# Optimization experiments

Measured on AMD Instinct MI355X. Metric: run time of the kernel, lower is better.

## Reference

```python
import jax, jax.numpy as jnp
import numpy as np

C = 128; HEADS = 8; GH = 32; GW = 32; B = 8; PD = 8  # PD = (dim//4)//4

def _conv(x, w, pad, dil=1, groups=1):
    return jax.lax.conv_general_dilated(
        x, w, (1, 1), [(pad[0], pad[0]), (pad[1], pad[1])],
        rhs_dilation=(dil, dil),
        dimension_numbers=('NCHW', 'OIHW', 'NCHW'),
        feature_group_count=groups)

def _lrelu(t):
    return jnp.where(t >= 0, t, 0.1 * t)

def _ln(t, g, b, eps=1e-5):
    m = jnp.mean(t, -1, keepdims=True)
    v = jnp.var(t, -1, keepdims=True)
    return (t - m) * jax.lax.rsqrt(v + eps) * g + b

def setup_inputs():
    rng = np.random.RandomState(0)
    f = lambda *s: jnp.asarray((rng.randn(*s) * 0.05).astype(np.float32))
    ones = lambda n: jnp.ones((n,), jnp.float32)
    zeros = lambda n: jnp.zeros((n,), jnp.float32)
    # Swin-style relative position index over the (GH, GW) group
    coords = np.stack(np.meshgrid(np.arange(GH), np.arange(GW), indexing='ij')).reshape(2, -1)
    rel = (coords[:, :, None] - coords[:, None, :]).transpose(1, 2, 0)
    rel[..., 0] += GH - 1; rel[..., 1] += GW - 1; rel[..., 0] *= 2 * GW - 1
    rel_idx = jnp.asarray(rel.sum(-1).astype(np.int32))  # [N, N]
    biases = np.stack(np.meshgrid(np.arange(1 - GH, GH), np.arange(1 - GW, GW), indexing='ij'))
    biases = jnp.asarray(biases.reshape(2, -1).T.astype(np.float32))  # [(2GH-1)*(2GW-1), 2]
    return dict(
        x=jnp.asarray(rng.rand(B, C, GH, GW).astype(np.float32)),
        conv1_w=f(C, C, 3, 3), conv2_w=f(C, C, 3, 3), conv3_w=f(C, C, 3, 3),
        convt_w=f(C, 3, 1, 1),
        rba_w=f(C, C, 3, 1), rba_b=zeros(C), rbb_w=f(C, C, 1, 3), rbb_b=zeros(C),
        pp_w=f(PD, 2), pp_b=zeros(PD),
        l1_g=ones(PD), l1_b=zeros(PD), l1_w=f(PD, PD), l1_b2=zeros(PD),
        l2_g=ones(PD), l2_b=zeros(PD), l2_w=f(PD, PD), l2_b2=zeros(PD),
        l3_g=ones(PD), l3_b=zeros(PD), l3_w=f(HEADS, PD), l3_b2=zeros(HEADS),
        qk_w=f(2 * C, C), qk_b=zeros(2 * C),
        v_w=f(C, C), v_b=zeros(C),
        proj_w=f(C, C), proj_b=zeros(C),
        fc1_w=f(C, C), fc1_b=zeros(C), fc2_w=f(C, C), fc2_b=zeros(C),
        biases=biases, rel_idx=rel_idx,
    )

def reference(x, conv1_w, conv2_w, conv3_w, convt_w, rba_w, rba_b, rbb_w, rbb_b,
              pp_w, pp_b, l1_g, l1_b, l1_w, l1_b2, l2_g, l2_b, l2_w, l2_b2,
              l3_g, l3_b, l3_w, l3_b2, qk_w, qk_b, v_w, v_b, proj_w, proj_b,
              fc1_w, fc1_b, fc2_w, fc2_b, biases, rel_idx):
    Bn, Cc, Hh, Ww = x.shape
    N = Hh * Ww
    hd = Cc // HEADS
    # FeaExtract: ResASPP (3 dilated 3x3 convs, grouped 1x1 merge) + residual
    b1 = _lrelu(_conv(x, conv1_w, (1, 1)))
    b2 = _lrelu(_conv(x, conv2_w, (3, 3), dil=3))
    b3 = _lrelu(_conv(x, conv3_w, (5, 5), dil=5))
    a = _conv(jnp.concatenate([b1, b2, b3], 1), convt_w, (0, 0), groups=Cc) + x
    # RB: (3,1) conv -> lrelu -> (1,3) conv + residual
    r = _lrelu(_conv(a, rba_w, (1, 0)) + rba_b[None, :, None, None])
    r = _conv(r, rbb_w, (0, 1)) + rbb_b[None, :, None, None]
    o0 = r + a
    # original uses in-place clamp_, so o0 is clamped before flattening
    o0 = jnp.clip(o0, 0.0, 1.0)
    E = o0.reshape(Bn, Cc, N).transpose(0, 2, 1)  # [B, N, C]
    qk = E @ qk_w.T + qk_b  # [B, N, 2C]
    q = qk[..., :Cc].reshape(Bn, N, HEADS, hd).transpose(0, 2, 1, 3)
    k = qk[..., Cc:].reshape(Bn, N, HEADS, hd).transpose(0, 2, 1, 3)
    v = (E @ v_w.T + v_b).reshape(Bn, N, HEADS, hd).transpose(0, 2, 1, 3)
    attn = jnp.einsum('bhid,bhjd->bhij', q * (hd ** -0.5), k)
    # DynamicPosBias MLP (residual=False): Linear(2,pd) -> [LN,ReLU,Linear] x2 -> LN,ReLU,Linear(pd,heads)
    p = biases @ pp_w.T + pp_b
    p = jax.nn.relu(_ln(p, l1_g, l1_b)) @ l1_w.T + l1_b2
    p = jax.nn.relu(_ln(p, l2_g, l2_b)) @ l2_w.T + l2_b2
    p = jax.nn.relu(_ln(p, l3_g, l3_b)) @ l3_w.T + l3_b2  # [L, heads]
    rpb = p[rel_idx]  # gather -> [N, N, heads]
    attn = attn + rpb.transpose(2, 0, 1)[None]
    attn = jax.nn.softmax(attn, axis=-1)
    y = jnp.einsum('bhij,bhjd->bhid', attn, v).transpose(0, 2, 1, 3).reshape(Bn, N, Cc) + E
    x_proj = y @ proj_w.T + proj_b
    h = jax.nn.gelu(x_proj @ fc1_w.T + fc1_b, approximate=False)
    return (h @ fc2_w.T + fc2_b) + y
```

## Files before the change

### kernel.cpp

```cpp
#include <hip/hip_runtime.h>
#include <hip/hip_bf16.h>

typedef __hip_bfloat16 bf16;
typedef __bf16 bf16x8 __attribute__((ext_vector_type(8)));
typedef float f32x4 __attribute__((ext_vector_type(4)));
typedef __fp16 f16x2 __attribute__((ext_vector_type(2)));
typedef __fp16 f16x4 __attribute__((ext_vector_type(4)));

#define Lb 3969
#define LOG2E 1.4426950408889634f
#define EXP2(x) __builtin_amdgcn_exp2f(x)

#define XP_F   0
#define WF_F   903168
#define WR_F   1124352
#define WG_F   1173504
#define BH_F   1222656
#define QKV_F  1222656
#define AP_F   2795520
#define YT_F   2795520
#define EB_F   3352576
#define RPB_F  3876864
#define FLAG_F 3908616
#define RT_F   3908624
#define VT_F   4924432

__device__ __forceinline__ float b2f(bf16 v) { return __bfloat162float(v); }
__device__ __forceinline__ bf16 f2b(float v) { return __float2bfloat16(v); }

template <typename T> __device__ __forceinline__ float ldw(const void* p, int i);
template <> __device__ __forceinline__ float ldw<bf16>(const void* p, int i) {
  return __bfloat162float(((const bf16*)p)[i]);
}
template <> __device__ __forceinline__ float ldw<float>(const void* p, int i) {
  return ((const float*)p)[i];
}
template <typename T> __device__ __forceinline__ void stw(void* p, size_t i, float v);
template <> __device__ __forceinline__ void stw<bf16>(void* p, size_t i, float v) {
  ((bf16*)p)[i] = __float2bfloat16(v);
}
template <> __device__ __forceinline__ void stw<float>(void* p, size_t i, float v) {
  ((float*)p)[i] = v;
}

__device__ __forceinline__ unsigned pkh(float a, float b) {
  f16x2 t = __builtin_amdgcn_cvt_pkrtz(a, b);
  return *(unsigned*)&t;
}

__device__ __forceinline__ bool detect_local(const unsigned* x) {
  int lane = threadIdx.x & 63;
  int cnt = 0;
#pragma unroll
  for (int k = 0; k < 4; ++k) {
    unsigned lo = x[lane + 64 * k] & 0xFFFFu;
    cnt += (lo >= 0x3C00u && lo < 0x3F80u) ? 1 : 0;
  }
#pragma unroll
  for (int off = 1; off < 64; off <<= 1) cnt += __shfl_xor(cnt, off);
  return cnt >= 128;
}

template <typename T>
__device__ void wprep_all_body(const void* w1, const void* w2, const void* w3,
                               const void* rba_w, const void* rbb_w,
                               const void* qk_w, const void* v_w,
                               const void* proj_w, const void* fc1_w,
                               const void* fc2_w, bf16* __restrict__ Wf,
                               bf16* __restrict__ Wr, bf16* __restrict__ Wg)
{
  int tid = blockIdx.x * 256 + threadIdx.x;
  int lane = tid & 63, li = lane & 15, quad = lane >> 4;
  if (tid < 55296) {
    int mt = (tid >> 6) & 7;
    int Kc = (tid >> 9) & 3;
    int rem = tid >> 11;
    int t = rem % 9;
    int br = rem / 9;
    const void* w = (br == 0 ? w1 : (br == 1 ? w2 : w3));
    int o = mt * 16 + li;
    int ci0 = Kc * 32 + quad * 8;
#pragma unroll
    for (int j = 0; j < 8; ++j)
      Wf[(size_t)tid * 8 + j] = f2b(ldw<T>(w, (o * 128 + ci0 + j) * 9 + t));
  } else {
    int u = tid - 55296;
    if (u < 12288) {
      int Kc = (u >> 6) & 3, mt = (u >> 8) & 7, q = u >> 11;
      const void* w = (q >= 3) ? rbb_w : rba_w;
      int t = q % 3;
#pragma unroll
      for (int j = 0; j < 8; ++j)
        Wr[(size_t)u * 8 + j] =
            f2b(ldw<T>(w, ((mt * 16 + li) * 128 + Kc * 32 + quad * 8 + j) * 3 + t));
    } else if (u < 24576) {
      int g = u - 12288;
      int Kc = (g >> 6) & 3, mtg = g >> 8;
      const void* w; int mrow; float sc = 1.f;
      if (mtg < 16)      { w = qk_w;   mrow = mtg * 16;
                           if (mtg < 8) sc = 0.25f * LOG2E; }
      else if (mtg < 24) { w = v_w;    mrow = (mtg - 16) * 16; }
      else if (mtg < 32) { w = proj_w; mrow = (mtg - 24) * 16; }
      else if (mtg < 40) { w = fc1_w;  mrow = (mtg - 32) * 16; }
      else               { w = fc2_w;  mrow = (mtg - 40) * 16; }
#pragma unroll
      for (int j = 0; j < 8; ++j)
        Wg[(size_t)g * 8 + j] =
            f2b(sc * ldw<T>(w, (mrow + li) * 128 + Kc * 32 + quad * 8 + j));
    }
  }
}

template <typename T>
__device__ void nhwc_body(const void* x, bf16* __restrict__ xp,
                          bf16 (*tile)[128], int bid)
{
  const int b = bid >> 5;
  const int row = bid & 31;
  const int t = threadIdx.x;
  const size_t bbase = (size_t)b * 42 * 42 * 128;
  const bf16x8 z = (bf16x8){};

  if (t < 160) {
    int side = t / 80;
    int off = (t % 80) * 8;
    *(bf16x8*)&xp[bbase + ((size_t)(row + 5) * 42 + side * 37) * 128 + off] = z;
  }
  {
    int zr = (row < 5) ? row : ((row >= 27) ? row + 10 : -1);
    if (zr >= 0) {
      size_t base = bbase + (size_t)zr * 42 * 128;
      for (int k = t; k < 672; k += 256) *(bf16x8*)&xp[base + k * 8] = z;
    }
  }

  {
    int ci = t >> 1, half = t & 1;
#pragma unroll
    for (int j = 0; j < 16; ++j) {
      int px = half * 16 + j;
      tile[px][ci] = f2b(ldw<T>(x, ((size_t)b * 128 + ci) * 1024 + row * 32 + px));
    }
  }
  __syncthreads();
  {
    int px = t >> 3, c0 = (t & 7) * 16;
    bf16* dst = xp + (bbase + ((size_t)(row + 5) * 42 + (px + 5)) * 128 + c0);
#pragma unroll
    for (int j = 0; j < 16; ++j) dst[j] = tile[px][c0 + j];
  }
}

__global__ __launch_bounds__(256) void prep_kernel(
    const unsigned* x, const void* w1, const void* w2, const void* w3,
    const void* rba_w, const void* rbb_w, const void* qk_w, const void* v_w,
    const void* proj_w, const void* fc1_w, const void* fc2_w,
    bf16* Wf, bf16* Wr, bf16* Wg, bf16* xp, int* flag)
{
  __shared__ bf16 tile[32][128];
  bool isbf = detect_local(x);
  if (blockIdx.x < 312) {
    if (blockIdx.x == 0 && threadIdx.x == 0) *flag = isbf ? 1 : 0;
    if (isbf) wprep_all_body<bf16>(w1, w2, w3, rba_w, rbb_w, qk_w, v_w, proj_w,
                                   fc1_w, fc2_w, Wf, Wr, Wg);
    else      wprep_all_body<float>(w1, w2, w3, rba_w, rbb_w, qk_w, v_w, proj_w,
                                    fc1_w, fc2_w, Wf, Wr, Wg);
  } else {
    int bid = blockIdx.x - 312;
    if (isbf) nhwc_body<bf16>(x, xp, tile, bid);
    else      nhwc_body<float>(x, xp, tile, bid);
  }
}

__global__ __launch_bounds__(256) void aspp2_kernel(
    const bf16* __restrict__ xp, const bf16* __restrict__ Wf,
    bf16* __restrict__ bh)
{
  const int nt_ = blockIdx.x, br = blockIdx.y >> 1, mh = blockIdx.y & 1;
  const int bb = blockIdx.z;
  const int w = threadIdx.x >> 6, lane = threadIdx.x & 63;
  const int quad = lane >> 4, li = lane & 15;
  const int d = (br == 0 ? 1 : (br == 1 ? 3 : 5));
  const int pxw = nt_ * 64 + w * 16;
  const int y = pxw >> 5, xb = pxw & 31;

  f32x4 acc[4] = {};
  const bf16* Wbase = Wf + (size_t)br * 18432 * 8 + (size_t)mh * 4 * 64 * 8;

  for (int t = 0; t < 9; ++t) {
    const int dy = (t / 3 - 1) * d, dx = (t % 3 - 1) * d;
    const bf16* Asite =
        xp + (((size_t)bb * 42 + (y + 5 + dy)) * 42 + (xb + li + 5 + dx)) * 128;
    const bf16* Wt = Wbase + (size_t)t * 2048 * 8;
#pragma unroll
    for (int Kc = 0; Kc < 4; ++Kc) {
      bf16x8 afrag = *(const bf16x8*)(Asite + Kc * 32 + quad * 8);
      const bf16* Wk = Wt + (size_t)Kc * 512 * 8 + (size_t)lane * 8;
#pragma unroll
      for (int mt = 0; mt < 4; ++mt) {
        bf16x8 wfrag = *(const bf16x8*)(Wk + (size_t)mt * 64 * 8);
        acc[mt] = __builtin_amdgcn_mfma_f32_16x16x32_bf16(afrag, wfrag, acc[mt],
                                                          0, 0, 0);
      }
    }
  }
#pragma unroll
  for (int mt = 0; mt < 4; ++mt)
#pragma unroll
    for (int r = 0; r < 4; ++r) {
      int px = pxw + quad * 4 + r;
      bh[((size_t)bb * 1024 + px) * 384 + br * 128 + (mh * 4 + mt) * 16 + li] =
          f2b(acc[mt][r]);
    }
}

template <typename T>
__device__ void merge2_body(const bf16* __restrict__ xp, const void* wt,
                            const bf16* __restrict__ bh, bf16* __restrict__ ap,
                            float* cw)
{
  const int b = blockIdx.y, px0 = blockIdx.x * 32;
  const bf16x8 z = (bf16x8){};
  if (blockIdx.x == 0) {
    size_t base = ((size_t)b * 34 + 0) * 32 * 128;
    for (int k = threadIdx.x; k < 512; k += 256) *(bf16x8*)&ap[base + k * 8] = z;
  } else if (blockIdx.x == 31) {
    size_t base = ((size_t)b * 34 + 33) * 32 * 128;
    for (int k = threadIdx.x; k < 512; k += 256) *(bf16x8*)&ap[base + k * 8] = z;
  }
  for (int i = threadIdx.x; i < 384; i += 256) cw[i] = ldw<T>(wt, i);
  __syncthreads();
  const int pxl = threadIdx.x >> 3, og = threadIdx.x & 7;
  const int px = px0 + pxl, o0 = og * 16;
  const int y = px >> 5, x = px & 31;
  const bf16* brow = bh + ((size_t)b * 1024 + px) * 384 + o0 * 3;
  const bf16* xrow = xp + (((size_t)b * 42 + y + 5) * 42 + x + 5) * 128 + o0;
  bf16* arow = ap + (((size_t)b * 34 + y + 1) * 32 + x) * 128 + o0;

  bf16 bl[48], xl[16], ol[16];
#pragma unroll
  for (int k = 0; k < 6; ++k) *(bf16x8*)&bl[k * 8] = *(const bf16x8*)&brow[k * 8];
  *(bf16x8*)&xl[0] = *(const bf16x8*)&xrow[0];
  *(bf16x8*)&xl[8] = *(const bf16x8*)&xrow[8];
#pragma unroll
  for (int j = 0; j < 16; ++j) {
    float v = b2f(xl[j]);
#pragma unroll
    for (int i = 0; i < 3; ++i) {
      float t = b2f(bl[j * 3 + i]);
      v += cw[(o0 + j) * 3 + i] * (t >= 0.f ? t : 0.1f * t);
    }
    ol[j] = f2b(v);
  }
  *(bf16x8*)&arow[0] = *(bf16x8*)&ol[0];
  *(bf16x8*)&arow[8] = *(bf16x8*)&ol[8];
}

__global__ __launch_bounds__(256) void merge2_kernel(
    const bf16* xp, const void* wt, const bf16* bh, bf16* ap, const int* flag)
{
  __shared__ float cw[384];
  if (*flag) merge2_body<bf16>(xp, wt, bh, ap, cw);
  else       merge2_body<float>(xp, wt, bh, ap, cw);
}

template <typename T>
__device__ void rbf_body(const bf16* __restrict__ ap, const bf16* __restrict__ Wr,
                         const void* rba_b, const void* rbb_b,
                         bf16* __restrict__ Eb, bf16 (*r1row)[136])
{
  const int y = blockIdx.x, b = blockIdx.y;
  const int w = threadIdx.x >> 6, lane = threadIdx.x & 63;
  const int mh = w & 1, xb = (w >> 1) * 16;
  const int quad = lane >> 4, li = lane & 15;

  if (threadIdx.x < 128) {
    r1row[0][threadIdx.x] = f2b(0.f);
    r1row[33][threadIdx.x] = f2b(0.f);
  }

  f32x4 acc[4] = {};
#pragma unroll
  for (int t = 0; t < 3; ++t) {
    const bf16* Asite = ap + (((size_t)b * 34 + y + t) * 32 + xb + li) * 128;
#pragma unroll
    for (int Kc = 0; Kc < 4; ++Kc) {
      bf16x8 afrag = *(const bf16x8*)(Asite + Kc * 32 + quad * 8);
#pragma unroll
      for (int mt = 0; mt < 4; ++mt) {
        int f = (t * 8 + mh * 4 + mt) * 4 + Kc;
        bf16x8 wfrag = *(const bf16x8*)(Wr + ((size_t)f * 64 + lane) * 8);
        acc[mt] = __builtin_amdgcn_mfma_f32_16x16x32_bf16(afrag, wfrag, acc[mt],
                                                          0, 0, 0);
      }
    }
  }
#pragma unroll
  for (int mt = 0; mt < 4; ++mt) {
    int o = (mh * 4 + mt) * 16 + li;
    float bv = ldw<T>(rba_b, o);
#pragma unroll
    for (int r = 0; r < 4; ++r) {
      int x = xb + quad * 4 + r;
      float v = acc[mt][r] + bv;
      r1row[x + 1][o] = f2b(v >= 0.f ? v : 0.1f * v);
    }
  }
  __syncthreads();

  f32x4 acc2[4] = {};
#pragma unroll
  for (int t = 0; t < 3; ++t) {
#pragma unroll
    for (int Kc = 0; Kc < 4; ++Kc) {
      bf16x8 afrag = *(const bf16x8*)&r1row[xb + li + t][Kc * 32 + quad * 8];
#pragma unroll
      for (int mt = 0; mt < 4; ++mt) {
        int f = ((3 + t) * 8 + mh * 4 + mt) * 4 + Kc;
        bf16x8 wfrag = *(const bf16x8*)(Wr + ((size_t)f * 64 + lane) * 8);
        acc2[mt] = __builtin_amdgcn_mfma_f32_16x16x32_bf16(afrag, wfrag,
                                                           acc2[mt], 0, 0, 0);
      }
    }
  }
#pragma unroll
  for (int mt = 0; mt < 4; ++mt) {
    int o = (mh * 4 + mt) * 16 + li;
    float bv = ldw<T>(rbb_b, o);
#pragma unroll
    for (int r = 0; r < 4; ++r) {
      int x = xb + quad * 4 + r;
      float v = acc2[mt][r] + bv +
                b2f(ap[(((size_t)b * 34 + y + 1) * 32 + x) * 128 + o]);
      v = fminf(fmaxf(v, 0.f), 1.f);
      Eb[((size_t)b * 1024 + y * 32 + x) * 128 + o] = f2b(v);
    }
  }
}

__global__ __launch_bounds__(256) void rbf_kernel(
    const bf16* ap, const bf16* Wr, const void* rba_b, const void* rbb_b,
    bf16* Eb, const int* flag)
{
  __shared__ bf16 r1row[34][136];
  if (*flag) rbf_body<bf16>(ap, Wr, rba_b, rbb_b, Eb, r1row);
  else       rbf_body<float>(ap, Wr, rba_b, rbb_b, Eb, r1row);
}

template <typename T>
__device__ __forceinline__ void ln_relu8(const float* t, float* u,
                                         const void* g, const void* bb)
{
  float m = 0.f;
#pragma unroll
  for (int k = 0; k < 8; ++k) m += t[k];
  m *= 0.125f;
  float v = 0.f;
#pragma unroll
  for (int k = 0; k < 8; ++k) { float d = t[k] - m; v += d * d; }
  v *= 0.125f;
  float r = rsqrtf(v + 1e-5f);
#pragma unroll
  for (int k = 0; k < 8; ++k) {
    float val = (t[k] - m) * r * ldw<T>(g, k) + ldw<T>(bb, k);
    u[k] = val > 0.f ? val : 0.f;
  }
}

template <typename T>
__device__ __forceinline__ float dpb_one(
    int r, int h, const void* biases, const void* pp_w, const void* pp_b,
    const void* l1_g, const void* l1_b, const void* l1_w, const void* l1_b2,
    const void* l2_g, const void* l2_b, const void* l2_w, const void* l2_b2,
    const void* l3_g, const void* l3_b, const void* l3_w, const void* l3_b2)
{
  float b0 = ldw<T>(biases, r * 2), b1 = ldw<T>(biases, r * 2 + 1);
  float t[8], u[8];
#pragma unroll
  for (int j = 0; j < 8; ++j)
    t[j] = b0 * ldw<T>(pp_w, j * 2) + b1 * ldw<T>(pp_w, j * 2 + 1) +
           ldw<T>(pp_b, j);
  ln_relu8<T>(t, u, l1_g, l1_b);
#pragma unroll
  for (int j = 0; j < 8; ++j) {
    float s = ldw<T>(l1_b2, j);
#pragma unroll
    for (int k = 0; k < 8; ++k) s += u[k] * ldw<T>(l1_w, j * 8 + k);
    t[j] = s;
  }
  ln_relu8<T>(t, u, l2_g, l2_b);
#pragma unroll
  for (int j = 0; j < 8; ++j) {
    float s = ldw<T>(l2_b2, j);
#pragma unroll
    for (int k = 0; k < 8; ++k) s += u[k] * ldw<T>(l2_w, j * 8 + k);
    t[j] = s;
  }
  ln_relu8<T>(t, u, l3_g, l3_b);
  float s = ldw<T>(l3_b2, h);
#pragma unroll
  for (int k = 0; k < 8; ++k) s += u[k] * ldw<T>(l3_w, h * 8 + k);
  return s;
}

template <typename T>
__device__ void dpbrt_body(
    const void* biases, const void* pp_w, const void* pp_b, const void* l1_g,
    const void* l1_b, const void* l1_w, const void* l1_b2, const void* l2_g,
    const void* l2_b, const void* l2_w, const void* l2_b2, const void* l3_g,
    const void* l3_b, const void* l3_w, const void* l3_b2,
    float* __restrict__ RTf, float (*rpl)[47])
{
  const int tt = blockIdx.x, h = blockIdx.y;
  const int t = tt >> 1, p = tt & 1;
  const int lane = threadIdx.x, quad = lane >> 4, li = lane & 15;

  for (int e = lane; e < 94; e += 64) {
    int row = t + e / 47;
    int col = p * 16 + e % 47;
    rpl[e / 47][e % 47] =
        dpb_one<T>(row * 63 + col, h, biases, pp_w, pp_b, l1_g, l1_b, l1_w,
                   l1_b2, l2_g, l2_b, l2_w, l2_b2, l3_g, l3_b, l3_w, l3_b2) *
        LOG2E;
  }
  __syncthreads();

  float* dst = RTf + ((size_t)(h * 124 + tt) * 4) * 256 + lane * 4;
#pragma unroll
  for (int mt = 0; mt < 4; ++mt) {
    f32x4 v;
#pragma unroll
    for (int r = 0; r < 4; ++r) {
      int j = mt * 16 + quad * 4 + r;
      v[r] = rpl[1 - (j >> 5)][li - (j & 31) + 31];
    }
    *(f32x4*)(dst + mt * 256) = v;
  }
}

__global__ __launch_bounds__(64) void dpbrt_kernel(
    const void* biases, const void* pp_w, const void* pp_b, const void* l1_g,
    const void* l1_b, const void* l1_w, const void* l1_b2, const void* l2_g,
    const void* l2_b, const void* l2_w, const void* l2_b2, const void* l3_g,
    const void* l3_b, const void* l3_w, const void* l3_b2, float* RTf,
    const int* flag)
{
  __shared__ float rpl[2][47];
  if (*flag)
    dpbrt_body<bf16>(biases, pp_w, pp_b, l1_g, l1_b, l1_w, l1_b2, l2_g, l2_b,
                     l2_w, l2_b2, l3_g, l3_b, l3_w, l3_b2, RTf, rpl);
  else
    dpbrt_body<float>(biases, pp_w, pp_b, l1_g, l1_b, l1_w, l1_b2, l2_g, l2_b,
                      l2_w, l2_b2, l3_g, l3_b, l3_w, l3_b2, RTf, rpl);
}

template <typename T>
__device__ void qkv_body(const bf16* __restrict__ Eb, const bf16* __restrict__ Wg,
                         const void* qk_b, const void* v_b,
                         bf16* __restrict__ QKV, uint2* __restrict__ VTh)
{
  const int grp = blockIdx.y, b = blockIdx.z;
  const int w = threadIdx.x >> 6, lane = threadIdx.x & 63;
  const int quad = lane >> 4, li = lane & 15;
  const int pxw = blockIdx.x * 64 + w * 16;
  bf16x8 ef[4];
#pragma unroll
  for (int Kc = 0; Kc < 4; ++Kc)
    ef[Kc] = *(const bf16x8*)&Eb[((size_t)b * 1024 + pxw + li) * 128 + Kc * 32 +
                                 quad * 8];
  f32x4 acc[8] = {};
#pragma unroll
  for (int nt = 0; nt < 8; ++nt) {
    int g = grp * 8 + nt;
#pragma unroll
    for (int Kc = 0; Kc < 4; ++Kc) {
      bf16x8 wf = *(const bf16x8*)&Wg[(((size_t)g * 4 + Kc) * 64 + lane) * 8];
      acc[nt] = __builtin_amdgcn_mfma_f32_16x16x32_bf16(ef[Kc], wf, acc[nt],
                                                        0, 0, 0);
    }
  }
  if (grp < 2) {
#pragma unroll
    for (int nt = 0; nt < 8; ++nt) {
      int g = grp * 8 + nt;
      int o = g * 16 + li;
      float bv = (g < 8) ? (0.25f * LOG2E) * ldw<T>(qk_b, o) : ldw<T>(qk_b, o);
#pragma unroll
      for (int r = 0; r < 4; ++r) {
        int px = pxw + quad * 4 + r;
        QKV[((size_t)b * 1024 + px) * 384 + o] = f2b(acc[nt][r] + bv);
      }
    }
  } else {
#pragma unroll
    for (int nt = 0; nt < 8; ++nt) {
      int hh = nt;
      float bv = ldw<T>(v_b, nt * 16 + li);
      uint2 pu;
      pu.x = pkh(acc[nt][0] + bv, acc[nt][1] + bv);
      pu.y = pkh(acc[nt][2] + bv, acc[nt][3] + bv);
      VTh[(((size_t)(b * 8 + hh) * 16 + blockIdx.x) * 4 + w) * 64 + lane] = pu;
    }
  }
}

__global__ __launch_bounds__(256) void qkv_kernel(
    const bf16* Eb, const bf16* Wg, const void* qk_b, const void* v_b,
    bf16* QKV, uint2* VTh, const int* flag)
{
  if (*flag) qkv_body<bf16>(Eb, Wg, qk_b, v_b, QKV, VTh);
  else       qkv_body<float>(Eb, Wg, qk_b, v_b, QKV, VTh);
}

template <typename T>
__device__ void mlpf_body(const bf16* __restrict__ Yt, const bf16* __restrict__ Wg,
                          const void* proj_b, const void* fc1_b,
                          const void* fc2_b, void* out,
                          bf16 (*buf0)[136], bf16 (*buf1)[136])
{
  const int w = threadIdx.x >> 6, lane = threadIdx.x & 63;
  const int quad = lane >> 4, li = lane & 15;
  const size_t row0 = (size_t)blockIdx.x * 16;

  bf16x8 ef[4];
  f32x4 acc[2];

#pragma unroll
  for (int Kc = 0; Kc < 4; ++Kc)
    ef[Kc] = *(const bf16x8*)&Yt[(row0 + li) * 128 + Kc * 32 + quad * 8];
  acc[0] = (f32x4){}; acc[1] = (f32x4){};
#pragma unroll
  for (int j = 0; j < 2; ++j) {
    int g = 24 + w * 2 + j;
#pragma unroll
    for (int Kc = 0; Kc < 4; ++Kc) {
      bf16x8 wf = *(const bf16x8*)&Wg[(((size_t)g * 4 + Kc) * 64 + lane) * 8];
      acc[j] = __builtin_amdgcn_mfma_f32_16x16x32_bf16(ef[Kc], wf, acc[j],
                                                       0, 0, 0);
    }
  }
#pragma unroll
  for (int j = 0; j < 2; ++j) {
    int o = (w * 2 + j) * 16 + li;
    float bv = ldw<T>(proj_b, o);
#pragma unroll
    for (int r = 0; r < 4; ++r)
      buf0[quad * 4 + r][o] = f2b(acc[j][r] + bv);
  }
  __syncthreads();

#pragma unroll
  for (int Kc = 0; Kc < 4; ++Kc)
    ef[Kc] = *(const bf16x8*)&buf0[li][Kc * 32 + quad * 8];
  acc[0] = (f32x4){}; acc[1] = (f32x4){};
#pragma unroll
  for (int j = 0; j < 2; ++j) {
    int g = 32 + w * 2 + j;
#pragma unroll
    for (int Kc = 0; Kc < 4; ++Kc) {
      bf16x8 wf = *(const bf16x8*)&Wg[(((size_t)g * 4 + Kc) * 64 + lane) * 8];
      acc[j] = __builtin_amdgcn_mfma_f32_16x16x32_bf16(ef[Kc], wf, acc[j],
                                                       0, 0, 0);
    }
  }
#pragma unroll
  for (int j = 0; j < 2; ++j) {
    int o = (w * 2 + j) * 16 + li;
    float bv = ldw<T>(fc1_b, o);
#pragma unroll
    for (int r = 0; r < 4; ++r) {
      float v = acc[j][r] + bv;
      v = 0.5f * v * (1.f + erff(v * 0.70710678118f));
      buf1[quad * 4 + r][o] = f2b(v);
    }
  }
  __syncthreads();

#pragma unroll
  for (int Kc = 0; Kc < 4; ++Kc)
    ef[Kc] = *(const bf16x8*)&buf1[li][Kc * 32 + quad * 8];
  acc[0] = (f32x4){}; acc[1] = (f32x4){};
#pragma unroll
  for (int j = 0; j < 2; ++j) {
    int g = 40 + w * 2 + j;
#pragma unroll
    for (int Kc = 0; Kc < 4; ++Kc) {
      bf16x8 wf = *(const bf16x8*)&Wg[(((size_t)g * 4 + Kc) * 64 + lane) * 8];
      acc[j] = __builtin_amdgcn_mfma_f32_16x16x32_bf16(ef[Kc], wf, acc[j],
                                                       0, 0, 0);
    }
  }
#pragma unroll
  for (int j = 0; j < 2; ++j) {
    int o = (w * 2 + j) * 16 + li;
    float bv = ldw<T>(fc2_b, o);
#pragma unroll
    for (int r = 0; r < 4; ++r) {
      size_t oidx = (row0 + quad * 4 + r) * 128 + o;
      float v = acc[j][r] + bv + b2f(Yt[oidx]);
      stw<T>(out, oidx, v);
    }
  }
}

__global__ __launch_bounds__(256) void mlpf_kernel(
    const bf16* Yt, const bf16* Wg, const void* proj_b, const void* fc1_b,
    const void* fc2_b, void* out, const int* flag)
{
  __shared__ bf16 buf0[16][136];
  __shared__ bf16 buf1[16][136];
  if (*flag) mlpf_body<bf16>(Yt, Wg, proj_b, fc1_b, fc2_b, out, buf0, buf1);
  else       mlpf_body<float>(Yt, Wg, proj_b, fc1_b, fc2_b, out, buf0, buf1);
}

__global__ __launch_bounds__(256, 4) void attn_kernel(
    const bf16* __restrict__ QKV, const bf16* __restrict__ Eb,
    const float* __restrict__ RTf, const uint2* __restrict__ VTh,
    bf16* __restrict__ Yt)
{
  const int qt = blockIdx.x * 4 + (threadIdx.x >> 6);
  const int hh = blockIdx.y;
  const int b = blockIdx.z;

  const int lane = threadIdx.x & 63;
  const int quad = lane >> 4, li = lane & 15;
  const int qb = qt * 16;

  const bf16* QKVb = QKV + (size_t)b * 1024 * 384;
  const uint2* VTb = VTh + (size_t)(b * 8 + hh) * 4096;
  const float* RTh = RTf + (size_t)hh * 124 * 1024;

  bf16x8 qf = (bf16x8){};
  if (quad < 2)
    qf = *(const bf16x8*)&QKVb[(size_t)(qb + li) * 384 + hh * 16 + quad * 8];

  f32x4 Oa = {}, Ob = {};
  float m_st = -1e30f, l_ln = 0.f;
  const int sbase = (lane & 48) + ((lane >> 2) & 12);

  struct Buf { bf16x8 kf[4]; f32x4 cin[4]; uint2 vb[4]; };
  Buf bA, bB;

  auto LOAD = [&](Buf& bf, int c) {
    const int c0 = c * 64;
    const int tt = ((qt >> 1) - 2 * c + 30) * 2 + (qt & 1);
    const float* rtp = RTh + (size_t)tt * 1024 + lane * 4;
#pragma unroll
    for (int mt = 0; mt < 4; ++mt) {
      bf.cin[mt] = *(const f32x4*)(rtp + mt * 256);
      bf.kf[mt] = (bf16x8){};
      if (quad < 2)
        bf.kf[mt] = *(const bf16x8*)&QKVb[(size_t)(c0 + mt * 16 + li) * 384 +
                                          128 + hh * 16 + quad * 8];
      bf.vb[mt] = VTb[(size_t)(c * 4 + mt) * 64 + lane];
    }
  };

  auto STEP = [&](const Buf& bf) {
    f32x4 sT[4];
#pragma unroll
    for (int mt = 0; mt < 4; ++mt)
      sT[mt] = __builtin_amdgcn_mfma_f32_16x16x32_bf16(bf.kf[mt], qf,
                                                       bf.cin[mt], 0, 0, 0);

    float m0 = fmaxf(fmaxf(sT[0][0], sT[0][1]), fmaxf(sT[0][2], sT[0][3]));
    float m1 = fmaxf(fmaxf(sT[1][0], sT[1][1]), fmaxf(sT[1][2], sT[1][3]));
    float m2 = fmaxf(fmaxf(sT[2][0], sT[2][1]), fmaxf(sT[2][2], sT[2][3]));
    float m3 = fmaxf(fmaxf(sT[3][0], sT[3][1]), fmaxf(sT[3][2], sT[3][3]));
    float lmax = fmaxf(fmaxf(m0, m1), fmaxf(m2, m3));

    if (!__all(lmax <= m_st + 11.5f)) {
      float cm = fmaxf(lmax, __shfl_xor(lmax, 16));
      cm = fmaxf(cm, __shfl_xor(cm, 32));
      float mn = fmaxf(m_st, cm);
      float al = EXP2(m_st - mn);
      m_st = mn;
      l_ln *= al;
#pragma unroll
      for (int r = 0; r < 4; ++r) {
        float a = __shfl(al, sbase + r);
        Oa[r] *= a;
        Ob[r] *= a;
      }
    }

#pragma unroll
    for (int mt = 0; mt < 4; ++mt)
#pragma unroll
      for (int r = 0; r < 4; ++r) sT[mt][r] = EXP2(sT[mt][r] - m_st);

    float s0 = (sT[0][0] + sT[0][1]) + (sT[0][2] + sT[0][3]);
    float s1 = (sT[1][0] + sT[1][1]) + (sT[1][2] + sT[1][3]);
    float s2 = (sT[2][0] + sT[2][1]) + (sT[2][2] + sT[2][3]);
    float s3 = (sT[3][0] + sT[3][1]) + (sT[3][2] + sT[3][3]);
    l_ln += (s0 + s1) + (s2 + s3);

#pragma unroll
    for (int mt = 0; mt < 4; ++mt) {
      union { unsigned u[2]; f16x4 h4; } pu;
      pu.u[0] = pkh(sT[mt][0], sT[mt][1]);
      pu.u[1] = pkh(sT[mt][2], sT[mt][3]);
      union { uint2 u; f16x4 h; } vu;
      vu.u = bf.vb[mt];
      if (mt & 2)
        Ob = __builtin_amdgcn_mfma_f32_16x16x16f16(pu.h4, vu.h, Ob, 0, 0, 0);
      else
        Oa = __builtin_amdgcn_mfma_f32_16x16x16f16(pu.h4, vu.h, Oa, 0, 0, 0);
    }
  };

  LOAD(bA, 0);
  for (int c = 0; c < 16; c += 2) {
    LOAD(bB, c + 1);
    STEP(bA);
    if (c + 2 < 16) LOAD(bA, c + 2);
    STEP(bB);
  }

  float l_st = l_ln + __shfl_xor(l_ln, 16);
  l_st += __shfl_xor(l_st, 32);

  f32x4 O_;
#pragma unroll
  for (int r = 0; r < 4; ++r) O_[r] = Oa[r] + Ob[r];

  const bf16* Ebp = Eb + (size_t)b * 1024 * 128 + hh * 16 + li;
  bf16* Ytp = Yt + (size_t)b * 1024 * 128 + hh * 16 + li;
#pragma unroll
  for (int r = 0; r < 4; ++r) {
    float lb = __shfl(l_st, sbase + r);
    int qrow = qb + quad * 4 + r;
    Ytp[(size_t)qrow * 128] =
        f2b(O_[r] / lb + b2f(Ebp[(size_t)qrow * 128]));
  }
}

extern "C" void kernel_launch(void* const* d_in, const int* in_sizes, int n_in,
                              void* d_out, int out_size, void* d_ws,
                              size_t ws_size, hipStream_t stream)
{
  (void)in_sizes; (void)n_in; (void)out_size; (void)ws_size;
  const void* x       = d_in[0];
  const void* conv1_w = d_in[1];
  const void* conv2_w = d_in[2];
  const void* conv3_w = d_in[3];
  const void* convt_w = d_in[4];
  const void* rba_w   = d_in[5];
  const void* rba_b   = d_in[6];
  const void* rbb_w   = d_in[7];
  const void* rbb_b   = d_in[8];
  const void* pp_w    = d_in[9];
  const void* pp_b    = d_in[10];
  const void* l1_g    = d_in[11];
  const void* l1_b    = d_in[12];
  const void* l1_w    = d_in[13];
  const void* l1_b2   = d_in[14];
  const void* l2_g    = d_in[15];
  const void* l2_b    = d_in[16];
  const void* l2_w    = d_in[17];
  const void* l2_b2   = d_in[18];
  const void* l3_g    = d_in[19];
  const void* l3_b    = d_in[20];
  const void* l3_w    = d_in[21];
  const void* l3_b2   = d_in[22];
  const void* qk_w    = d_in[23];
  const void* qk_b    = d_in[24];
  const void* v_w     = d_in[25];
  const void* v_b     = d_in[26];
  const void* proj_w  = d_in[27];
  const void* proj_b  = d_in[28];
  const void* fc1_w   = d_in[29];
  const void* fc1_b   = d_in[30];
  const void* fc2_w   = d_in[31];
  const void* fc2_b   = d_in[32];
  const void* biases  = d_in[33];

  float* ws   = (float*)d_ws;
  bf16*  xp   = (bf16*)(ws + XP_F);
  bf16*  Wf   = (bf16*)(ws + WF_F);
  bf16*  Wr   = (bf16*)(ws + WR_F);
  bf16*  Wg   = (bf16*)(ws + WG_F);
  bf16*  bh   = (bf16*)(ws + BH_F);
  bf16*  QKV  = (bf16*)(ws + QKV_F);
  bf16*  ap   = (bf16*)(ws + AP_F);
  bf16*  Yt   = (bf16*)(ws + YT_F);
  bf16*  Eb   = (bf16*)(ws + EB_F);
  int*   flag = (int*)(ws + FLAG_F);
  float* RTf  = ws + RT_F;
  uint2* VTh  = (uint2*)(ws + VT_F);

  prep_kernel<<<568, 256, 0, stream>>>(
      (const unsigned*)x, conv1_w, conv2_w, conv3_w, rba_w, rbb_w, qk_w, v_w,
      proj_w, fc1_w, fc2_w, Wf, Wr, Wg, xp, flag);
  aspp2_kernel<<<dim3(16, 6, 8), 256, 0, stream>>>(xp, Wf, bh);
  merge2_kernel<<<dim3(32, 8), 256, 0, stream>>>(xp, convt_w, bh, ap, flag);
  rbf_kernel<<<dim3(32, 8), 256, 0, stream>>>(ap, Wr, rba_b, rbb_b, Eb, flag);
  dpbrt_kernel<<<dim3(124, 8), 64, 0, stream>>>(
      biases, pp_w, pp_b, l1_g, l1_b, l1_w, l1_b2, l2_g, l2_b, l2_w, l2_b2,
      l3_g, l3_b, l3_w, l3_b2, RTf, flag);
  qkv_kernel<<<dim3(16, 3, 8), 256, 0, stream>>>(Eb, Wg, qk_b, v_b, QKV, VTh,
                                                 flag);
  attn_kernel<<<dim3(16, 8, 8), 256, 0, stream>>>(QKV, Eb, RTf, VTh, Yt);
  mlpf_kernel<<<512, 256, 0, stream>>>(Yt, Wg, proj_b, fc1_b, fc2_b, d_out,
                                       flag);
}
```

Measured before the change: 229.3 us.

## Fuse ASPP conv with merge and fold position-bias MLP into prep kernel

```diff
diff --git a/kernel.cpp b/kernel.cpp
--- a/kernel.cpp
+++ b/kernel.cpp
@@ -15,12 +15,10 @@
 #define WF_F   903168
 #define WR_F   1124352
 #define WG_F   1173504
-#define BH_F   1222656
 #define QKV_F  1222656
 #define AP_F   2795520
 #define YT_F   2795520
 #define EB_F   3352576
-#define RPB_F  3876864
 #define FLAG_F 3908616
 #define RT_F   3908624
 #define VT_F   4924432
@@ -59,6 +57,62 @@
 #pragma unroll
   for (int off = 1; off < 64; off <<= 1) cnt += __shfl_xor(cnt, off);
   return cnt >= 128;
+}
+
+template <typename T>
+__device__ __forceinline__ void ln_relu8(const float* t, float* u,
+                                         const void* g, const void* bb)
+{
+  float m = 0.f;
+#pragma unroll
+  for (int k = 0; k < 8; ++k) m += t[k];
+  m *= 0.125f;
+  float v = 0.f;
+#pragma unroll
+  for (int k = 0; k < 8; ++k) { float d = t[k] - m; v += d * d; }
+  v *= 0.125f;
+  float r = rsqrtf(v + 1e-5f);
+#pragma unroll
+  for (int k = 0; k < 8; ++k) {
+    float val = (t[k] - m) * r * ldw<T>(g, k) + ldw<T>(bb, k);
+    u[k] = val > 0.f ? val : 0.f;
+  }
+}
+
+template <typename T>
+__device__ __forceinline__ float dpb_one(
+    int r, int h, const void* biases, const void* pp_w, const void* pp_b,
+    const void* l1_g, const void* l1_b, const void* l1_w, const void* l1_b2,
+    const void* l2_g, const void* l2_b, const void* l2_w, const void* l2_b2,
+    const void* l3_g, const void* l3_b, const void* l3_w, const void* l3_b2)
+{
+  float b0 = ldw<T>(biases, r * 2), b1 = ldw<T>(biases, r * 2 + 1);
+  float t[8], u[8];
+#pragma unroll
+  for (int j = 0; j < 8; ++j)
+    t[j] = b0 * ldw<T>(pp_w, j * 2) + b1 * ldw<T>(pp_w, j * 2 + 1) +
+           ldw<T>(pp_b, j);
+  ln_relu8<T>(t, u, l1_g, l1_b);
+#pragma unroll
+  for (int j = 0; j < 8; ++j) {
+    float s = ldw<T>(l1_b2, j);
+#pragma unroll
+    for (int k = 0; k < 8; ++k) s += u[k] * ldw<T>(l1_w, j * 8 + k);
+    t[j] = s;
+  }
+  ln_relu8<T>(t, u, l2_g, l2_b);
+#pragma unroll
+  for (int j = 0; j < 8; ++j) {
+    float s = ldw<T>(l2_b2, j);
+#pragma unroll
+    for (int k = 0; k < 8; ++k) s += u[k] * ldw<T>(l2_w, j * 8 + k);
+    t[j] = s;
+  }
+  ln_relu8<T>(t, u, l3_g, l3_b);
+  float s = ldw<T>(l3_b2, h);
+#pragma unroll
+  for (int k = 0; k < 8; ++k) s += u[k] * ldw<T>(l3_w, h * 8 + k);
+  return s;
 }
 
 template <typename T>
@@ -151,13 +205,50 @@
   }
 }
 
+template <typename T>
+__device__ void dpbrt_wave(
+    int tt, int h, int lane, const void* biases, const void* pp_w,
+    const void* pp_b, const void* l1_g, const void* l1_b, const void* l1_w,
+    const void* l1_b2, const void* l2_g, const void* l2_b, const void* l2_w,
+    const void* l2_b2, const void* l3_g, const void* l3_b, const void* l3_w,
+    const void* l3_b2, float* __restrict__ RTf, float (*rp)[47])
+{
+  const int t = tt >> 1, p = tt & 1;
+  const int quad = lane >> 4, li = lane & 15;
+  for (int e = lane; e < 94; e += 64) {
+    int row = t + e / 47;
+    int col = p * 16 + e % 47;
+    rp[e / 47][e % 47] =
+        dpb_one<T>(row * 63 + col, h, biases, pp_w, pp_b, l1_g, l1_b, l1_w,
+                   l1_b2, l2_g, l2_b, l2_w, l2_b2, l3_g, l3_b, l3_w, l3_b2) *
+        LOG2E;
+  }
+  __syncthreads();
+  float* dst = RTf + ((size_t)(h * 124 + tt) * 4) * 256 + lane * 4;
+#pragma unroll
+  for (int mt = 0; mt < 4; ++mt) {
+    f32x4 v;
+#pragma unroll
+    for (int r = 0; r < 4; ++r) {
+      int j = mt * 16 + quad * 4 + r;
+      v[r] = rp[1 - (j >> 5)][li - (j & 31) + 31];
+    }
+    *(f32x4*)(dst + mt * 256) = v;
+  }
+}
+
 __global__ __launch_bounds__(256) void prep_kernel(
     const unsigned* x, const void* w1, const void* w2, const void* w3,
     const void* rba_w, const void* rbb_w, const void* qk_w, const void* v_w,
     const void* proj_w, const void* fc1_w, const void* fc2_w,
-    bf16* Wf, bf16* Wr, bf16* Wg, bf16* xp, int* flag)
+    bf16* Wf, bf16* Wr, bf16* Wg, bf16* xp, int* flag,
+    const void* biases, const void* pp_w, const void* pp_b, const void* l1_g,
+    const void* l1_b, const void* l1_w, const void* l1_b2, const void* l2_g,
+    const void* l2_b, const void* l2_w, const void* l2_b2, const void* l3_g,
+    const void* l3_b, const void* l3_w, const void* l3_b2, float* RTf)
 {
   __shared__ bf16 tile[32][128];
+  __shared__ float rpl[4][2][47];
   bool isbf = detect_local(x);
   if (blockIdx.x < 312) {
     if (blockIdx.x == 0 && threadIdx.x == 0) *flag = isbf ? 1 : 0;
@@ -165,103 +256,112 @@
                                    fc1_w, fc2_w, Wf, Wr, Wg);
     else      wprep_all_body<float>(w1, w2, w3, rba_w, rbb_w, qk_w, v_w, proj_w,
                                     fc1_w, fc2_w, Wf, Wr, Wg);
-  } else {
+  } else if (blockIdx.x < 568) {
     int bid = blockIdx.x - 312;
     if (isbf) nhwc_body<bf16>(x, xp, tile, bid);
     else      nhwc_body<float>(x, xp, tile, bid);
-  }
-}
-
-__global__ __launch_bounds__(256) void aspp2_kernel(
-    const bf16* __restrict__ xp, const bf16* __restrict__ Wf,
-    bf16* __restrict__ bh)
-{
-  const int nt_ = blockIdx.x, br = blockIdx.y >> 1, mh = blockIdx.y & 1;
-  const int bb = blockIdx.z;
+  } else {
+    int wv = threadIdx.x >> 6, lane = threadIdx.x & 63;
+    int idx = (blockIdx.x - 568) * 4 + wv;
+    int tt = idx % 124, h = idx / 124;
+    if (isbf)
+      dpbrt_wave<bf16>(tt, h, lane, biases, pp_w, pp_b, l1_g, l1_b, l1_w,
+                       l1_b2, l2_g, l2_b, l2_w, l2_b2, l3_g, l3_b, l3_w,
+                       l3_b2, RTf, rpl[wv]);
+    else
+      dpbrt_wave<float>(tt, h, lane, biases, pp_w, pp_b, l1_g, l1_b, l1_w,
+                        l1_b2, l2_g, l2_b, l2_w, l2_b2, l3_g, l3_b, l3_w,
+                        l3_b2, RTf, rpl[wv]);
+  }
+}
+
+#define ASPP_SEG(BR, M8, DIL)                                                  \
+  {                                                                            \
+    for (int t = 0; t < 9; ++t) {                                              \
+      const int dy = (t / 3 - 1) * (DIL), dx = (t % 3 - 1) * (DIL);            \
+      const bf16* Asite =                                                      \
+          xp + (((size_t)bb * 42 + (y + 5 + dy)) * 42 + (xb + li + 5 + dx)) *  \
+                   128;                                                        \
+      const bf16* Wt2 = Wf + (((size_t)(BR)*9 + t) * 4) * 512 * 8;             \
+      _Pragma("unroll") for (int Kc = 0; Kc < 4; ++Kc) {                       \
+        bf16x8 afrag = *(const bf16x8*)(Asite + Kc * 32 + quad * 8);           \
+        const bf16* Wk = Wt2 + (size_t)Kc * 512 * 8 + (size_t)lane * 8;        \
+        _Pragma("unroll") for (int m = 0; m < 4; ++m) {                        \
+          bf16x8 wfrag = *(const bf16x8*)(Wk + (size_t)((M8) + m) * 64 * 8);   \
+          acc[m] = __builtin_amdgcn_mfma_f32_16x16x32_bf16(afrag, wfrag,       \
+                                                           acc[m], 0, 0, 0);   \
+        }                                                                      \
+      }                                                                        \
+    }                                                                          \
+  }
+
+template <typename T>
+__device__ void aspp_merge_body(const bf16* __restrict__ xp,
+                                const bf16* __restrict__ Wf, const void* wt,
+                                bf16* __restrict__ ap, bf16 (*conc)[200],
+                                float* cw)
+{
+  const int nt_ = blockIdx.x, mh = blockIdx.y, bb = blockIdx.z;
   const int w = threadIdx.x >> 6, lane = threadIdx.x & 63;
   const int quad = lane >> 4, li = lane & 15;
-  const int d = (br == 0 ? 1 : (br == 1 ? 3 : 5));
-  const int pxw = nt_ * 64 + w * 16;
+  const int pxw = nt_ * 16;
   const int y = pxw >> 5, xb = pxw & 31;
 
+  if (mh == 0 && (nt_ == 0 || nt_ == 63)) {
+    const bf16x8 z = (bf16x8){};
+    size_t base = ((size_t)bb * 34 + (nt_ == 0 ? 0 : 33)) * 32 * 128;
+    for (int k = threadIdx.x; k < 512; k += 192) *(bf16x8*)&ap[base + k * 8] = z;
+  }
+  if (threadIdx.x < 192) cw[threadIdx.x] = ldw<T>(wt, mh * 192 + threadIdx.x);
+
   f32x4 acc[4] = {};
-  const bf16* Wbase = Wf + (size_t)br * 18432 * 8 + (size_t)mh * 4 * 64 * 8;
-
-  for (int t = 0; t < 9; ++t) {
-    const int dy = (t / 3 - 1) * d, dx = (t % 3 - 1) * d;
-    const bf16* Asite =
-        xp + (((size_t)bb * 42 + (y + 5 + dy)) * 42 + (xb + li + 5 + dx)) * 128;
-    const bf16* Wt = Wbase + (size_t)t * 2048 * 8;
-#pragma unroll
-    for (int Kc = 0; Kc < 4; ++Kc) {
-      bf16x8 afrag = *(const bf16x8*)(Asite + Kc * 32 + quad * 8);
-      const bf16* Wk = Wt + (size_t)Kc * 512 * 8 + (size_t)lane * 8;
-#pragma unroll
-      for (int mt = 0; mt < 4; ++mt) {
-        bf16x8 wfrag = *(const bf16x8*)(Wk + (size_t)mt * 64 * 8);
-        acc[mt] = __builtin_amdgcn_mfma_f32_16x16x32_bf16(afrag, wfrag, acc[mt],
-                                                          0, 0, 0);
+  const int seg = mh * 3 + w;
+  if (seg == 0)      ASPP_SEG(0, 0, 1)
+  else if (seg == 1) ASPP_SEG(0, 4, 1)
+  else if (seg == 2) ASPP_SEG(1, 0, 3)
+  else if (seg == 3) ASPP_SEG(1, 4, 3)
+  else if (seg == 4) ASPP_SEG(2, 0, 5)
+  else               ASPP_SEG(2, 4, 5)
+
+#pragma unroll
+  for (int mt = 0; mt < 4; ++mt)
+#pragma unroll
+    for (int r = 0; r < 4; ++r)
+      conc[quad * 4 + r][(w * 4 + mt) * 16 + li] = f2b(acc[mt][r]);
+  __syncthreads();
+
+  if (threadIdx.x < 128) {
+    const int pxl = threadIdx.x >> 3;
+    const int o0 = (threadIdx.x & 7) * 8;
+    const int px = pxw + pxl;
+    const int yy = px >> 5, xx = px & 31;
+    const bf16* xrow =
+        xp + (((size_t)bb * 42 + yy + 5) * 42 + xx + 5) * 128 + mh * 64 + o0;
+    bf16* arow =
+        ap + (((size_t)bb * 34 + yy + 1) * 32 + xx) * 128 + mh * 64 + o0;
+    bf16 xl[8], ol[8];
+    *(bf16x8*)&xl[0] = *(const bf16x8*)&xrow[0];
+#pragma unroll
+    for (int j = 0; j < 8; ++j) {
+      float v = b2f(xl[j]);
+#pragma unroll
+      for (int i = 0; i < 3; ++i) {
+        float t = b2f(conc[pxl][(o0 + j) * 3 + i]);
+        v += cw[(o0 + j) * 3 + i] * (t >= 0.f ? t : 0.1f * t);
       }
-    }
-  }
-#pragma unroll
-  for (int mt = 0; mt < 4; ++mt)
-#pragma unroll
-    for (int r = 0; r < 4; ++r) {
-      int px = pxw + quad * 4 + r;
-      bh[((size_t)bb * 1024 + px) * 384 + br * 128 + (mh * 4 + mt) * 16 + li] =
-          f2b(acc[mt][r]);
-    }
-}
-
-template <typename T>
-__device__ void merge2_body(const bf16* __restrict__ xp, const void* wt,
-                            const bf16* __restrict__ bh, bf16* __restrict__ ap,
-                            float* cw)
-{
-  const int b = blockIdx.y, px0 = blockIdx.x * 32;
-  const bf16x8 z = (bf16x8){};
-  if (blockIdx.x == 0) {
-    size_t base = ((size_t)b * 34 + 0) * 32 * 128;
-    for (int k = threadIdx.x; k < 512; k += 256) *(bf16x8*)&ap[base + k * 8] = z;
-  } else if (blockIdx.x == 31) {
-    size_t base = ((size_t)b * 34 + 33) * 32 * 128;
-    for (int k = threadIdx.x; k < 512; k += 256) *(bf16x8*)&ap[base + k * 8] = z;
-  }
-  for (int i = threadIdx.x; i < 384; i += 256) cw[i] = ldw<T>(wt, i);
-  __syncthreads();
-  const int pxl = threadIdx.x >> 3, og = threadIdx.x & 7;
-  const int px = px0 + pxl, o0 = og * 16;
-  const int y = px >> 5, x = px & 31;
-  const bf16* brow = bh + ((size_t)b * 1024 + px) * 384 + o0 * 3;
-  const bf16* xrow = xp + (((size_t)b * 42 + y + 5) * 42 + x + 5) * 128 + o0;
-  bf16* arow = ap + (((size_t)b * 34 + y + 1) * 32 + x) * 128 + o0;
-
-  bf16 bl[48], xl[16], ol[16];
-#pragma unroll
-  for (int k = 0; k < 6; ++k) *(bf16x8*)&bl[k * 8] = *(const bf16x8*)&brow[k * 8];
-  *(bf16x8*)&xl[0] = *(const bf16x8*)&xrow[0];
-  *(bf16x8*)&xl[8] = *(const bf16x8*)&xrow[8];
-#pragma unroll
-  for (int j = 0; j < 16; ++j) {
-    float v = b2f(xl[j]);
-#pragma unroll
-    for (int i = 0; i < 3; ++i) {
-      float t = b2f(bl[j * 3 + i]);
-      v += cw[(o0 + j) * 3 + i] * (t >= 0.f ? t : 0.1f * t);
-    }
-    ol[j] = f2b(v);
-  }
-  *(bf16x8*)&arow[0] = *(bf16x8*)&ol[0];
-  *(bf16x8*)&arow[8] = *(bf16x8*)&ol[8];
-}
-
-__global__ __launch_bounds__(256) void merge2_kernel(
-    const bf16* xp, const void* wt, const bf16* bh, bf16* ap, const int* flag)
-{
-  __shared__ float cw[384];
-  if (*flag) merge2_body<bf16>(xp, wt, bh, ap, cw);
-  else       merge2_body<float>(xp, wt, bh, ap, cw);
+      ol[j] = f2b(v);
+    }
+    *(bf16x8*)&arow[0] = *(bf16x8*)&ol[0];
+  }
+}
+
+__global__ __launch_bounds__(192) void aspp_merge_kernel(
+    const bf16* xp, const bf16* Wf, const void* wt, bf16* ap, const int* flag)
+{
+  __shared__ bf16 conc[16][200];
+  __shared__ float cw[192];
+  if (*flag) aspp_merge_body<bf16>(xp, Wf, wt, ap, conc, cw);
+  else       aspp_merge_body<float>(xp, Wf, wt, ap, conc, cw);
 }
 
 template <typename T>
@@ -345,113 +445,6 @@
   __shared__ bf16 r1row[34][136];
   if (*flag) rbf_body<bf16>(ap, Wr, rba_b, rbb_b, Eb, r1row);
   else       rbf_body<float>(ap, Wr, rba_b, rbb_b, Eb, r1row);
-}
-
-template <typename T>
-__device__ __forceinline__ void ln_relu8(const float* t, float* u,
-                                         const void* g, const void* bb)
-{
-  float m = 0.f;
-#pragma unroll
-  for (int k = 0; k < 8; ++k) m += t[k];
-  m *= 0.125f;
-  float v = 0.f;
-#pragma unroll
-  for (int k = 0; k < 8; ++k) { float d = t[k] - m; v += d * d; }
-  v *= 0.125f;
-  float r = rsqrtf(v + 1e-5f);
-#pragma unroll
-  for (int k = 0; k < 8; ++k) {
-    float val = (t[k] - m) * r * ldw<T>(g, k) + ldw<T>(bb, k);
-    u[k] = val > 0.f ? val : 0.f;
-  }
-}
-
-template <typename T>
-__device__ __forceinline__ float dpb_one(
-    int r, int h, const void* biases, const void* pp_w, const void* pp_b,
-    const void* l1_g, const void* l1_b, const void* l1_w, const void* l1_b2,
-    const void* l2_g, const void* l2_b, const void* l2_w, const void* l2_b2,
-    const void* l3_g, const void* l3_b, const void* l3_w, const void* l3_b2)
-{
-  float b0 = ldw<T>(biases, r * 2), b1 = ldw<T>(biases, r * 2 + 1);
-  float t[8], u[8];
-#pragma unroll
-  for (int j = 0; j < 8; ++j)
-    t[j] = b0 * ldw<T>(pp_w, j * 2) + b1 * ldw<T>(pp_w, j * 2 + 1) +
-           ldw<T>(pp_b, j);
-  ln_relu8<T>(t, u, l1_g, l1_b);
-#pragma unroll
-  for (int j = 0; j < 8; ++j) {
-    float s = ldw<T>(l1_b2, j);
-#pragma unroll
-    for (int k = 0; k < 8; ++k) s += u[k] * ldw<T>(l1_w, j * 8 + k);
-    t[j] = s;
-  }
-  ln_relu8<T>(t, u, l2_g, l2_b);
-#pragma unroll
-  for (int j = 0; j < 8; ++j) {
-    float s = ldw<T>(l2_b2, j);
-#pragma unroll
-    for (int k = 0; k < 8; ++k) s += u[k] * ldw<T>(l2_w, j * 8 + k);
-    t[j] = s;
-  }
-  ln_relu8<T>(t, u, l3_g, l3_b);
-  float s = ldw<T>(l3_b2, h);
-#pragma unroll
-  for (int k = 0; k < 8; ++k) s += u[k] * ldw<T>(l3_w, h * 8 + k);
-  return s;
-}
-
-template <typename T>
-__device__ void dpbrt_body(
-    const void* biases, const void* pp_w, const void* pp_b, const void* l1_g,
-    const void* l1_b, const void* l1_w, const void* l1_b2, const void* l2_g,
-    const void* l2_b, const void* l2_w, const void* l2_b2, const void* l3_g,
-    const void* l3_b, const void* l3_w, const void* l3_b2,
-    float* __restrict__ RTf, float (*rpl)[47])
-{
-  const int tt = blockIdx.x, h = blockIdx.y;
-  const int t = tt >> 1, p = tt & 1;
-  const int lane = threadIdx.x, quad = lane >> 4, li = lane & 15;
-
-  for (int e = lane; e < 94; e += 64) {
-    int row = t + e / 47;
-    int col = p * 16 + e % 47;
-    rpl[e / 47][e % 47] =
-        dpb_one<T>(row * 63 + col, h, biases, pp_w, pp_b, l1_g, l1_b, l1_w,
-                   l1_b2, l2_g, l2_b, l2_w, l2_b2, l3_g, l3_b, l3_w, l3_b2) *
-        LOG2E;
-  }
-  __syncthreads();
-
-  float* dst = RTf + ((size_t)(h * 124 + tt) * 4) * 256 + lane * 4;
-#pragma unroll
-  for (int mt = 0; mt < 4; ++mt) {
-    f32x4 v;
-#pragma unroll
-    for (int r = 0; r < 4; ++r) {
-      int j = mt * 16 + quad * 4 + r;
-      v[r] = rpl[1 - (j >> 5)][li - (j & 31) + 31];
-    }
-    *(f32x4*)(dst + mt * 256) = v;
-  }
-}
-
-__global__ __launch_bounds__(64) void dpbrt_kernel(
-    const void* biases, const void* pp_w, const void* pp_b, const void* l1_g,
-    const void* l1_b, const void* l1_w, const void* l1_b2, const void* l2_g,
-    const void* l2_b, const void* l2_w, const void* l2_b2, const void* l3_g,
-    const void* l3_b, const void* l3_w, const void* l3_b2, float* RTf,
-    const int* flag)
-{
-  __shared__ float rpl[2][47];
-  if (*flag)
-    dpbrt_body<bf16>(biases, pp_w, pp_b, l1_g, l1_b, l1_w, l1_b2, l2_g, l2_b,
-                     l2_w, l2_b2, l3_g, l3_b, l3_w, l3_b2, RTf, rpl);
-  else
-    dpbrt_body<float>(biases, pp_w, pp_b, l1_g, l1_b, l1_w, l1_b2, l2_g, l2_b,
-                      l2_w, l2_b2, l3_g, l3_b, l3_w, l3_b2, RTf, rpl);
 }
 
 template <typename T>
@@ -780,7 +773,6 @@
   bf16*  Wf   = (bf16*)(ws + WF_F);
   bf16*  Wr   = (bf16*)(ws + WR_F);
   bf16*  Wg   = (bf16*)(ws + WG_F);
-  bf16*  bh   = (bf16*)(ws + BH_F);
   bf16*  QKV  = (bf16*)(ws + QKV_F);
   bf16*  ap   = (bf16*)(ws + AP_F);
   bf16*  Yt   = (bf16*)(ws + YT_F);
@@ -789,15 +781,14 @@
   float* RTf  = ws + RT_F;
   uint2* VTh  = (uint2*)(ws + VT_F);
 
-  prep_kernel<<<568, 256, 0, stream>>>(
+  prep_kernel<<<816, 256, 0, stream>>>(
       (const unsigned*)x, conv1_w, conv2_w, conv3_w, rba_w, rbb_w, qk_w, v_w,
-      proj_w, fc1_w, fc2_w, Wf, Wr, Wg, xp, flag);
-  aspp2_kernel<<<dim3(16, 6, 8), 256, 0, stream>>>(xp, Wf, bh);
-  merge2_kernel<<<dim3(32, 8), 256, 0, stream>>>(xp, convt_w, bh, ap, flag);
+      proj_w, fc1_w, fc2_w, Wf, Wr, Wg, xp, flag,
+      biases, pp_w, pp_b, l1_g, l1_b, l1_w, l1_b2, l2_g, l2_b, l2_w, l2_b2,
+      l3_g, l3_b, l3_w, l3_b2, RTf);
+  aspp_merge_kernel<<<dim3(64, 2, 8), 192, 0, stream>>>(xp, Wf, convt_w, ap,
+                                                        flag);
   rbf_kernel<<<dim3(32, 8), 256, 0, stream>>>(ap, Wr, rba_b, rbb_b, Eb, flag);
-  dpbrt_kernel<<<dim3(124, 8), 64, 0, stream>>>(
-      biases, pp_w, pp_b, l1_g, l1_b, l1_w, l1_b2, l2_g, l2_b, l2_w, l2_b2,
-      l3_g, l3_b, l3_w, l3_b2, RTf, flag);
   qkv_kernel<<<dim3(16, 3, 8), 256, 0, stream>>>(Eb, Wg, qk_b, v_b, QKV, VTh,
                                                  flag);
   attn_kernel<<<dim3(16, 8, 8), 256, 0, stream>>>(QKV, Eb, RTf, VTh, Yt);
```

Result: no change. 228.5 us, median of 2 (-0.4%).
